# Performance work log

Hardware: AMD Instinct MI355X
Metric: run time of the kernel (lower is better)

## Reference

```python
import jax, jax.numpy as jnp
import numpy as np

H = 768      # hidden size
F = 3072     # FFN intermediate (4*H)
E = 8        # num experts
K = 2        # top_k
B, S = 2, 2048


def setup_inputs() -> dict:
    key = jax.random.key(0)
    ks = jax.random.split(key, 6)
    scale_in = 1.0 / np.sqrt(H)
    scale_mid = 1.0 / np.sqrt(F)
    return {
        "x": jax.random.normal(ks[0], (B, S, H), dtype=jnp.float32),
        "gate_w": jax.random.normal(ks[1], (H, E), dtype=jnp.float32) * scale_in,
        "W1": jax.random.normal(ks[2], (E, H, F), dtype=jnp.float32) * scale_in,
        "b1": jnp.zeros((E, F), dtype=jnp.float32),
        "W2": jax.random.normal(ks[3], (E, F, H), dtype=jnp.float32) * scale_mid,
        "b2": jnp.zeros((E, H), dtype=jnp.float32),
    }


def reference(x, gate_w, W1, b1, W2, b2):
    """MoE FFN: top-k router -> per-expert FFN -> weighted combine.

    Faithful to the torch module: router logits = x @ gate_w (no bias),
    softmax over the top-k logits only, each expert is a dense FFN
    (Linear -> GELU -> Linear), output = sum_k w_k * expert_{idx_k}(x).
    Expressed densely: combine weights are scattered into a [T, E] matrix
    (zero for unselected experts), so running every expert on every token
    and contracting with the combine matrix yields identical math.
    """
    batch, seq_len, hidden = x.shape
    xf = x.reshape(-1, hidden)                       # [T, H]
    T = xf.shape[0]

    logits = xf @ gate_w                             # [T, E]
    top_w, top_idx = jax.lax.top_k(logits, K)        # [T, K]
    top_w = jax.nn.softmax(top_w, axis=-1)

    # scatter top-k softmax weights into dense [T, E] combine matrix
    comb = jnp.zeros((T, E), dtype=x.dtype).at[
        jnp.arange(T)[:, None], top_idx
    ].add(top_w)

    # all experts on all tokens (zero combine weight kills unselected)
    h = jnp.einsum('th,ehf->etf', xf, W1) + b1[:, None, :]   # [E, T, F]
    h = jax.nn.gelu(h)
    y = jnp.einsum('etf,efh->eth', h, W2) + b2[:, None, :]   # [E, T, H]

    out = jnp.einsum('te,eth->th', comb, y)                  # [T, H]
    return out.reshape(batch, seq_len, hidden)
```

## Files before the change

### kernel.cpp

```cpp
#include <hip/hip_runtime.h>

#define H 768
#define F 3072
#define NE 8
#define T 4096
#define NA 8192
#define TP 9216
#define NRB 72

typedef unsigned short ushort_t;
typedef __attribute__((ext_vector_type(8))) short bfx8;
typedef __attribute__((ext_vector_type(4))) float fx4;
typedef __attribute__((address_space(3))) const ushort_t lus;

__device__ __forceinline__ ushort_t f2bf(float f) {
    union { float f; unsigned u; } v; v.f = f;
    unsigned u = v.u;
    unsigned r = (u + 0x7fffu + ((u >> 16) & 1u)) >> 16;
    return (ushort_t)r;
}

__device__ __forceinline__ float gelu_tanh(float x) {
    const float c = 0.7978845608028654f;
    float z = c * (x + 0.044715f * x * x * x);
    float t = 1.0f - 2.0f / (__expf(2.0f * z) + 1.0f);
    return 0.5f * x * (1.0f + t);
}

__device__ __forceinline__ void g2l16(const void* g, void* l) {
    __builtin_amdgcn_global_load_lds(
        (__attribute__((address_space(1))) void*)g,
        (__attribute__((address_space(3))) void*)l, 16, 0, 0);
}

__device__ __forceinline__ bfx8 dsr128(lus* p) {
    bfx8 r;
    asm volatile("ds_read_b128 %0, %1" : "=v"(r) : "v"(p));
    return r;
}

#define WAITV0 asm volatile("s_waitcnt vmcnt(0)" ::: "memory")
#define LGKM8  asm volatile("s_waitcnt lgkmcnt(8)" ::: "memory")
#define LGKM0  asm volatile("s_waitcnt lgkmcnt(0)" ::: "memory")
#define SBAR   asm volatile("s_barrier" ::: "memory")
#define SCHED0 __builtin_amdgcn_sched_barrier(0)
#define PRIO1  __builtin_amdgcn_s_setprio(1)
#define PRIO0  __builtin_amdgcn_s_setprio(0)

__global__ void router_k(const float* __restrict__ x, const float* __restrict__ gw,
                         int* __restrict__ tidx, float* __restrict__ twgt) {
    int t = blockIdx.x * 4 + (threadIdx.x >> 6);
    int lane = threadIdx.x & 63;
    const float* xr = x + (size_t)t * H;
    float acc[NE];
#pragma unroll
    for (int e = 0; e < NE; ++e) acc[e] = 0.f;
    for (int h = lane; h < H; h += 64) {
        float xv = xr[h];
        const float* g = gw + h * NE;
#pragma unroll
        for (int e = 0; e < NE; ++e) acc[e] += xv * g[e];
    }
#pragma unroll
    for (int off = 32; off > 0; off >>= 1) {
#pragma unroll
        for (int e = 0; e < NE; ++e) acc[e] += __shfl_down(acc[e], off);
    }
    if (lane == 0) {
        float l0 = -1e30f, l1 = -1e30f; int i0 = 0, i1 = 0;
#pragma unroll
        for (int e = 0; e < NE; ++e) {
            float v = acc[e];
            if (v > l0) { l1 = l0; i1 = i0; l0 = v; i0 = e; }
            else if (v > l1) { l1 = v; i1 = e; }
        }
        float w0 = 1.f / (1.f + __expf(l1 - l0));
        tidx[t * 2] = i0; tidx[t * 2 + 1] = i1;
        twgt[t * 2] = w0; twgt[t * 2 + 1] = 1.f - w0;
    }
}

__global__ void init_k(int* counts, int* tos) {
    int i = blockIdx.x * 256 + threadIdx.x;
    if (i < NE) counts[i] = 0;
    if (i < TP) tos[i] = -1;
}

__global__ void count_k(const int* __restrict__ tidx, int* counts) {
    int i = blockIdx.x * 256 + threadIdx.x;
    if (i < NA) atomicAdd(&counts[tidx[i]], 1);
}

__global__ void offsets_k(const int* __restrict__ counts, int* cursor,
                          int* rbe, int* rbs) {
    int off = 0, rb = 0;
    for (int e = 0; e < NE; ++e) {
        cursor[e] = off;
        int nrb = (counts[e] + 127) / 128;
        for (int j = 0; j < nrb; ++j) { rbe[rb] = e; rbs[rb] = off + j * 128; ++rb; }
        off += nrb * 128;
    }
    for (; rb < NRB; ++rb) rbe[rb] = -1;
}

__global__ void scatter_k(const int* __restrict__ tidx, int* cursor,
                          int* __restrict__ tos, int* __restrict__ aslot) {
    int i = blockIdx.x * 256 + threadIdx.x;
    if (i < NA) {
        int e = tidx[i];
        int slot = atomicAdd(&cursor[e], 1);
        tos[slot] = i >> 1;
        aslot[i] = slot;
    }
}

__global__ void gather_k(const float* __restrict__ x, const int* __restrict__ tos,
                         ushort_t* __restrict__ xg) {
    int i = blockIdx.x * 256 + threadIdx.x;
    int slot = i / (H / 8);
    int j = i % (H / 8);
    int tok = tos[slot];
    ushort_t v[8];
    if (tok < 0) {
#pragma unroll
        for (int q = 0; q < 8; ++q) v[q] = 0;
    } else {
        const float* src = x + (size_t)tok * H + j * 8;
#pragma unroll
        for (int q = 0; q < 8; ++q) v[q] = f2bf(src[q]);
    }
    *(bfx8*)&xg[(size_t)slot * H + j * 8] = *(const bfx8*)v;
}

__global__ void transpose_cast_k(const float* __restrict__ src, ushort_t* __restrict__ dst,
                                 int R, int C) {
    int e = blockIdx.z;
    src += (size_t)e * R * C;
    dst += (size_t)e * R * C;
    int c0 = blockIdx.x * 64, r0 = blockIdx.y * 64;
    __shared__ float tile[64][65];
    int tid = threadIdx.x;
    int cc = tid & 63, rr = tid >> 6;
#pragma unroll
    for (int rep = 0; rep < 16; ++rep) {
        int r = rep * 4 + rr;
        tile[r][cc] = src[(size_t)(r0 + r) * C + c0 + cc];
    }
    __syncthreads();
#pragma unroll
    for (int rep = 0; rep < 16; ++rep) {
        int c = rep * 4 + rr;
        dst[(size_t)(c0 + c) * R + r0 + cc] = f2bf(tile[cc][c]);
    }
}

template <int DO_GELU>
__global__ __launch_bounds__(256, 3)
void gemm_tile_k(const ushort_t* __restrict__ A, const ushort_t* __restrict__ Bt,
                 const float* __restrict__ bias, void* __restrict__ Cout,
                 const int* __restrict__ rbe, const int* __restrict__ rbs,
                 int K, int N, int ncb) {
    int nwg = gridDim.x, bid = blockIdx.x;
    int wgid = (bid & 7) * (nwg >> 3) + (bid >> 3);
    int rb = wgid / ncb, cb = wgid % ncb;
    int e = rbe[rb];
    if (e < 0) return;
    int slot0 = rbs[rb];

    __shared__ __align__(16) ushort_t lds[16384];

    int tid = threadIdx.x, lane = tid & 63, wid = tid >> 6;
    int wm = wid >> 1, wn = wid & 1;
    int l15 = lane & 15, qh = lane >> 4, sw = l15 & 7;

    const ushort_t* Ab = A + (size_t)slot0 * K;
    const ushort_t* Bb = Bt + ((size_t)e * N + cb * 128) * K;

    int j = tid >> 3, q = tid & 7;
    int cs = (q ^ (j & 7)) * 8;
    int ldsw = wid * 512;
    const ushort_t* aSrc = Ab + (size_t)j * K + cs;
    const ushort_t* bSrc = Bb + (size_t)j * K + cs;

    int ch0 = (qh ^ sw) << 3;
    int ch1 = ((4 + qh) ^ sw) << 3;
    int abase = (wm * 64 + l15) * 64;
    int bbase = 8192 + (wn * 64 + l15) * 64;

#define STAGE_T(KT) do { \
    _Pragma("unroll") for (int u = 0; u < 4; ++u) \
        g2l16(aSrc + (size_t)u * 32 * K + (KT) * 64, &lds[u * 2048 + ldsw]); \
    _Pragma("unroll") for (int u = 0; u < 4; ++u) \
        g2l16(bSrc + (size_t)u * 32 * K + (KT) * 64, &lds[8192 + u * 2048 + ldsw]); \
} while (0)

    fx4 acc[4][4];
#pragma unroll
    for (int m = 0; m < 4; ++m)
#pragma unroll
        for (int n = 0; n < 4; ++n) acc[m][n] = (fx4){0.f, 0.f, 0.f, 0.f};
    bfx8 a0[4], a1[4], b0v[4], b1v[4];

    int NT = K >> 6;
    STAGE_T(0);

    for (int t = 0; t < NT; ++t) {
        WAITV0;
        SBAR;
#pragma unroll
        for (int m = 0; m < 4; ++m) a0[m] = dsr128((lus*)&lds[abase + m * 1024 + ch0]);
#pragma unroll
        for (int n = 0; n < 4; ++n) b0v[n] = dsr128((lus*)&lds[bbase + n * 1024 + ch0]);
#pragma unroll
        for (int m = 0; m < 4; ++m) a1[m] = dsr128((lus*)&lds[abase + m * 1024 + ch1]);
#pragma unroll
        for (int n = 0; n < 4; ++n) b1v[n] = dsr128((lus*)&lds[bbase + n * 1024 + ch1]);
        LGKM8; SCHED0;
        PRIO1;
#pragma unroll
        for (int m = 0; m < 4; ++m)
#pragma unroll
            for (int n = 0; n < 4; ++n)
                acc[m][n] = __builtin_amdgcn_mfma_f32_16x16x32_bf16(a0[m], b0v[n], acc[m][n], 0, 0, 0);
        PRIO0;
        LGKM0; SCHED0;
        PRIO1;
#pragma unroll
        for (int m = 0; m < 4; ++m)
#pragma unroll
            for (int n = 0; n < 4; ++n)
                acc[m][n] = __builtin_amdgcn_mfma_f32_16x16x32_bf16(a1[m], b1v[n], acc[m][n], 0, 0, 0);
        PRIO0;
        SBAR;
        if (t + 1 < NT) STAGE_T(t + 1);
    }
#undef STAGE_T

#pragma unroll
    for (int n = 0; n < 4; ++n) {
        int col = cb * 128 + wn * 64 + n * 16 + l15;
        float bvv = bias[(size_t)e * N + col];
#pragma unroll
        for (int m = 0; m < 4; ++m) {
            int rowb = slot0 + wm * 64 + m * 16 + qh * 4;
            fx4 v = acc[m][n];
#pragma unroll
            for (int jj = 0; jj < 4; ++jj) {
                float val = v[jj] + bvv;
                if (DO_GELU) {
                    ((ushort_t*)Cout)[(size_t)(rowb + jj) * N + col] = f2bf(gelu_tanh(val));
                } else {
                    ((float*)Cout)[(size_t)(rowb + jj) * N + col] = val;
                }
            }
        }
    }
}

__global__ void combine_k(const float* __restrict__ y, const int* __restrict__ aslot,
                          const float* __restrict__ twgt, float* __restrict__ out) {
    int i = blockIdx.x * 256 + threadIdx.x;
    int t = i / (H / 4);
    int j = i % (H / 4);
    int s0 = aslot[t * 2], s1 = aslot[t * 2 + 1];
    float w0 = twgt[t * 2], w1 = twgt[t * 2 + 1];
    const float4 a = ((const float4*)(y + (size_t)s0 * H))[j];
    const float4 b = ((const float4*)(y + (size_t)s1 * H))[j];
    float4 r;
    r.x = w0 * a.x + w1 * b.x;
    r.y = w0 * a.y + w1 * b.y;
    r.z = w0 * a.z + w1 * b.z;
    r.w = w0 * a.w + w1 * b.w;
    ((float4*)(out + (size_t)t * H))[j] = r;
}

extern "C" void kernel_launch(void* const* d_in, const int* in_sizes, int n_in,
                              void* d_out, int out_size, void* d_ws, size_t ws_size,
                              hipStream_t stream) {
    const float* x  = (const float*)d_in[0];
    const float* gw = (const float*)d_in[1];
    const float* W1 = (const float*)d_in[2];
    const float* b1 = (const float*)d_in[3];
    const float* W2 = (const float*)d_in[4];
    const float* b2 = (const float*)d_in[5];
    float* out = (float*)d_out;

    char* ws = (char*)d_ws;
    size_t o = 0;
    auto carve = [&](size_t bytes) -> void* {
        o = (o + 255) & ~(size_t)255;
        void* p = ws + o;
        o += bytes;
        return p;
    };
    int*      tidx   = (int*)carve((size_t)NA * 4);
    float*    twgt   = (float*)carve((size_t)NA * 4);
    int*      counts = (int*)carve(NE * 4);
    int*      cursor = (int*)carve(NE * 4);
    int*      rbe    = (int*)carve(NRB * 4);
    int*      rbs    = (int*)carve(NRB * 4);
    int*      aslot  = (int*)carve((size_t)NA * 4);
    int*      tos    = (int*)carve((size_t)TP * 4);
    ushort_t* xg     = (ushort_t*)carve((size_t)TP * H * 2);
    ushort_t* w1t    = (ushort_t*)carve((size_t)NE * H * F * 2);
    ushort_t* w2t    = (ushort_t*)carve((size_t)NE * H * F * 2);
    ushort_t* hbuf   = (ushort_t*)carve((size_t)TP * F * 2);
    float*    ybuf   = (float*)xg;
    (void)in_sizes; (void)n_in; (void)out_size; (void)ws_size;

    hipLaunchKernelGGL(init_k, dim3(TP / 256), dim3(256), 0, stream, counts, tos);
    hipLaunchKernelGGL(router_k, dim3(T / 4), dim3(256), 0, stream, x, gw, tidx, twgt);
    hipLaunchKernelGGL(count_k, dim3(NA / 256), dim3(256), 0, stream, tidx, counts);
    hipLaunchKernelGGL(offsets_k, dim3(1), dim3(1), 0, stream, counts, cursor, rbe, rbs);
    hipLaunchKernelGGL(scatter_k, dim3(NA / 256), dim3(256), 0, stream, tidx, cursor, tos, aslot);
    hipLaunchKernelGGL(gather_k, dim3(TP * (H / 8) / 256), dim3(256), 0, stream, x, tos, xg);
    hipLaunchKernelGGL(transpose_cast_k, dim3(F / 64, H / 64, NE), dim3(256), 0, stream, W1, w1t, H, F);
    hipLaunchKernelGGL(transpose_cast_k, dim3(H / 64, F / 64, NE), dim3(256), 0, stream, W2, w2t, F, H);
    hipLaunchKernelGGL((gemm_tile_k<1>), dim3(NRB * (F / 128)), dim3(256), 0, stream,
                       xg, w1t, b1, (void*)hbuf, rbe, rbs, H, F, F / 128);
    hipLaunchKernelGGL((gemm_tile_k<0>), dim3(NRB * (H / 128)), dim3(256), 0, stream,
                       hbuf, w2t, b2, (void*)ybuf, rbe, rbs, F, H, H / 128);
    hipLaunchKernelGGL(combine_k, dim3(T * (H / 4) / 256), dim3(256), 0, stream,
                       ybuf, aslot, twgt, out);
}
```

Before: 257.5 us.

## Double-buffer B tiles in LDS and load A fragments directly into registers

The grouped GEMM kernel now stages only the B (weight) tile through LDS, in two ping-pong buffers. The next tile's copy is issued before the current tile's MFMAs, so global loads overlap with compute and the trailing barrier goes away. A operands are loaded straight from global memory into registers with a one-tile-ahead register prefetch, which skips the LDS round trip for A. The cost is more VGPRs for the doubled A fragments, possibly lower occupancy, and uncoalesced per-lane 16-byte A loads. The unrolled pair of iterations assumes NT is even.

After: 512.6 us. 1.99x slower.

```diff
diff --git a/kernel.cpp b/kernel.cpp
--- a/kernel.cpp
+++ b/kernel.cpp
@@ -40,7 +40,6 @@
 }
 
 #define WAITV0 asm volatile("s_waitcnt vmcnt(0)" ::: "memory")
-#define LGKM8  asm volatile("s_waitcnt lgkmcnt(8)" ::: "memory")
 #define LGKM0  asm volatile("s_waitcnt lgkmcnt(0)" ::: "memory")
 #define SBAR   asm volatile("s_barrier" ::: "memory")
 #define SCHED0 __builtin_amdgcn_sched_barrier(0)
@@ -179,62 +178,70 @@
     int j = tid >> 3, q = tid & 7;
     int cs = (q ^ (j & 7)) * 8;
     int ldsw = wid * 512;
-    const ushort_t* aSrc = Ab + (size_t)j * K + cs;
     const ushort_t* bSrc = Bb + (size_t)j * K + cs;
 
     int ch0 = (qh ^ sw) << 3;
     int ch1 = ((4 + qh) ^ sw) << 3;
-    int abase = (wm * 64 + l15) * 64;
-    int bbase = 8192 + (wn * 64 + l15) * 64;
-
-#define STAGE_T(KT) do { \
+    int bbase = (wn * 64 + l15) * 64;
+
+    const ushort_t* ap[4];
+#pragma unroll
+    for (int m = 0; m < 4; ++m)
+        ap[m] = Ab + (size_t)(wm * 64 + m * 16 + l15) * K + qh * 8;
+
+#define STAGE_B(BUF, KT) do { \
     _Pragma("unroll") for (int u = 0; u < 4; ++u) \
-        g2l16(aSrc + (size_t)u * 32 * K + (KT) * 64, &lds[u * 2048 + ldsw]); \
-    _Pragma("unroll") for (int u = 0; u < 4; ++u) \
-        g2l16(bSrc + (size_t)u * 32 * K + (KT) * 64, &lds[8192 + u * 2048 + ldsw]); \
+        g2l16(bSrc + (size_t)u * 32 * K + (KT) * 64, &lds[(BUF) * 8192 + u * 2048 + ldsw]); \
 } while (0)
 
+#define LOADA(ARR) do { \
+    _Pragma("unroll") for (int m = 0; m < 4; ++m) { \
+        ARR[m * 2 + 0] = *(const bfx8*)(ap[m]); \
+        ARR[m * 2 + 1] = *(const bfx8*)(ap[m] + 32); \
+        ap[m] += 64; \
+    } \
+} while (0)
+
     fx4 acc[4][4];
 #pragma unroll
     for (int m = 0; m < 4; ++m)
 #pragma unroll
         for (int n = 0; n < 4; ++n) acc[m][n] = (fx4){0.f, 0.f, 0.f, 0.f};
-    bfx8 a0[4], a1[4], b0v[4], b1v[4];
+    bfx8 aA[8], aB[8], b0v[4], b1v[4];
 
     int NT = K >> 6;
-    STAGE_T(0);
-
-    for (int t = 0; t < NT; ++t) {
-        WAITV0;
-        SBAR;
-#pragma unroll
-        for (int m = 0; m < 4; ++m) a0[m] = dsr128((lus*)&lds[abase + m * 1024 + ch0]);
-#pragma unroll
-        for (int n = 0; n < 4; ++n) b0v[n] = dsr128((lus*)&lds[bbase + n * 1024 + ch0]);
-#pragma unroll
-        for (int m = 0; m < 4; ++m) a1[m] = dsr128((lus*)&lds[abase + m * 1024 + ch1]);
-#pragma unroll
-        for (int n = 0; n < 4; ++n) b1v[n] = dsr128((lus*)&lds[bbase + n * 1024 + ch1]);
-        LGKM8; SCHED0;
-        PRIO1;
-#pragma unroll
-        for (int m = 0; m < 4; ++m)
-#pragma unroll
-            for (int n = 0; n < 4; ++n)
-                acc[m][n] = __builtin_amdgcn_mfma_f32_16x16x32_bf16(a0[m], b0v[n], acc[m][n], 0, 0, 0);
-        PRIO0;
-        LGKM0; SCHED0;
-        PRIO1;
-#pragma unroll
-        for (int m = 0; m < 4; ++m)
-#pragma unroll
-            for (int n = 0; n < 4; ++n)
-                acc[m][n] = __builtin_amdgcn_mfma_f32_16x16x32_bf16(a1[m], b1v[n], acc[m][n], 0, 0, 0);
-        PRIO0;
-        SBAR;
-        if (t + 1 < NT) STAGE_T(t + 1);
-    }
-#undef STAGE_T
+    STAGE_B(0, 0);
+    LOADA(aA);
+
+#define ITER(BUF, ACUR, ANEXT, TT) do { \
+    WAITV0; \
+    SBAR; \
+    _Pragma("unroll") for (int n = 0; n < 4; ++n) \
+        b0v[n] = dsr128((lus*)&lds[(BUF) * 8192 + bbase + n * 1024 + ch0]); \
+    _Pragma("unroll") for (int n = 0; n < 4; ++n) \
+        b1v[n] = dsr128((lus*)&lds[(BUF) * 8192 + bbase + n * 1024 + ch1]); \
+    if ((TT) + 1 < NT) { \
+        STAGE_B(1 - (BUF), (TT) + 1); \
+        LOADA(ANEXT); \
+    } \
+    LGKM0; SCHED0; \
+    PRIO1; \
+    _Pragma("unroll") for (int m = 0; m < 4; ++m) \
+    _Pragma("unroll") for (int n = 0; n < 4; ++n) \
+        acc[m][n] = __builtin_amdgcn_mfma_f32_16x16x32_bf16(ACUR[m * 2 + 0], b0v[n], acc[m][n], 0, 0, 0); \
+    _Pragma("unroll") for (int m = 0; m < 4; ++m) \
+    _Pragma("unroll") for (int n = 0; n < 4; ++n) \
+        acc[m][n] = __builtin_amdgcn_mfma_f32_16x16x32_bf16(ACUR[m * 2 + 1], b1v[n], acc[m][n], 0, 0, 0); \
+    PRIO0; \
+} while (0)
+
+    for (int t = 0; t < NT; t += 2) {
+        ITER(0, aA, aB, t);
+        ITER(1, aB, aA, t + 1);
+    }
+#undef ITER
+#undef LOADA
+#undef STAGE_B
 
 #pragma unroll
     for (int n = 0; n < 4; ++n) {
```
